# Kernel optimization log

Hardware: AMD Instinct MI355X
Metric: run time of the kernel (lower is better)

The kernel has to match this reference:

```python
import jax, jax.numpy as jnp
import numpy as np

GAMMA = 0.7
ALPHA = 1.0
EPS = 1e-6

def setup_inputs() -> dict:
    key = jax.random.key(0)
    k1, k2 = jax.random.split(key)
    x = jax.random.normal(k1, (1, 4096, 1024), dtype=jnp.float32)
    attn = jax.random.uniform(k2, (1, 4096, 4096), dtype=jnp.float32)
    return {"x": x, "attn": attn, "layer_idx": 10, "total_layers": 12}


def reference(x, attn, layer_idx, total_layers):
    B, N, D = x.shape  # module's masking/cat logic requires B == 1
    if layer_idx < GAMMA * total_layers:
        return x

    # --- spatial autocorrelation score s ---
    a = x.mean(axis=-1)                                            # [B,N]
    z = (a - a.mean(1, keepdims=True)) / (a.std(1, ddof=1, keepdims=True) + EPS)
    # diag(z z^T * W) == z^2 * diag(W): skip the O(N^2) outer product
    I_l = z * z * jnp.diagonal(attn, axis1=-2, axis2=-1)           # [B,N]
    s = (I_l - I_l.mean(1, keepdims=True)) / (I_l.std(1, ddof=1, keepdims=True) + EPS)

    # --- threshold (torch.median returns the LOWER middle for even N) ---
    mu_s = s.mean(1, keepdims=True)
    abs_med = jnp.sort(jnp.abs(s), axis=1)[:, (N - 1) // 2][:, None]
    lb = ALPHA * (mu_s - abs_med)
    ub = ALPHA * (mu_s + abs_med)
    mask_A = (s < lb) | (s > ub)                                   # [B,N]

    xb = x[0]
    mA = mask_A[0]
    idx = jnp.arange(N)
    n_A = mA.sum()

    # compact A tokens to the front preserving original order
    orderA = jnp.argsort(~mA, stable=True)
    tokA = xb[orderA]                    # first n_A rows are tokens_A, rest are B tokens (masked later)
    mid = n_A // 2
    n2 = n_A - mid                       # number of A2 tokens

    # A1[i] = tokA[i] (valid i < mid); A2[j] = tokA[mid + j] (valid j < n2)
    A2 = jnp.take(tokA, jnp.clip(mid + idx, 0, N - 1), axis=0)     # [N,D] padded
    validA1 = idx < mid
    validA2 = idx < n2

    sim = tokA @ A2.T                                              # [N,N]
    sim = jnp.where(validA2[None, :], sim, -jnp.inf)
    matches = jnp.argmax(sim, axis=1)                              # [N]
    merged = 0.5 * (tokA + A2[matches])
    merged = jnp.where(validA1[:, None], merged, 0.0)              # rows >= mid zeroed

    # residual A2 tokens (not matched by any valid A1 row), compacted and zero-padded
    drop_idx = jnp.where(validA1, matches, N)                      # OOB index dropped
    matched = jnp.zeros(N, bool).at[drop_idx].set(True, mode='drop')
    resid_valid = validA2 & ~matched
    orderR = jnp.argsort(~resid_valid, stable=True)
    residual = jnp.where(resid_valid[orderR][:, None], A2[orderR], 0.0)  # [N,D]

    # B tokens compacted, then merged tokens appended, zero pad to N
    n_B = N - n_A
    orderB = jnp.argsort(mA, stable=True)
    tokB = jnp.where((idx < n_B)[:, None], xb[orderB], 0.0)        # [N,D]
    shift = jnp.clip(idx - n_B, 0, N - 1)
    in_merged = ((idx >= n_B) & (idx < n_B + mid)).astype(xb.dtype)[:, None]
    out = (tokB + in_merged * merged[shift])[None]                 # [1,N,D]
    return out, residual
```

## Files before the change

### kernel.cpp

```cpp
#include <hip/hip_runtime.h>

#define N 4096
#define D 1024
#define EPSF 1e-6f

typedef _Float16 f16;
typedef f16 f16x8 __attribute__((ext_vector_type(8)));
typedef float f32x4 __attribute__((ext_vector_type(4)));
typedef unsigned long long u64;

#define PLANE ((size_t)2048 * 1024)

struct WS {
  int n_A, mid, n2, n_B, n_resid, pad[3];
  float a[N];
  float diag[N];
  int A1idx[N];
  int A2idx[N];
  int Bidx[N];
  int matches[N];
  int residIdx[N];
  u64 bestKey[2048];
};

__device__ __forceinline__ u64 packKey(float v, int j) {
  unsigned u = __float_as_uint(v);
  unsigned m = (u & 0x80000000u) ? ~u : (u | 0x80000000u);
  return ((u64)m << 32) | (unsigned)(~(unsigned)j);
}

__global__ __launch_bounds__(256) void k_prep(const float* __restrict__ x,
                                              const float* __restrict__ attn, WS* ws) {
  int row = blockIdx.x;
  int t = threadIdx.x;
  float4 v = ((const float4*)(x + (size_t)row * D))[t];
  float sm = v.x + v.y + v.z + v.w;
  for (int o = 32; o; o >>= 1) sm += __shfl_down(sm, o, 64);
  __shared__ float w[4];
  if ((t & 63) == 0) w[t >> 6] = sm;
  __syncthreads();
  if (t == 0) {
    ws->a[row] = (w[0] + w[1] + w[2] + w[3]) * (1.0f / D);
    ws->diag[row] = attn[(size_t)row * N + row];
  }
}

__global__ __launch_bounds__(256) void k_mask(WS* ws) {
  __shared__ double dred[4], dred2[4];
  __shared__ float bcast[2];
  __shared__ int hist[256];
  __shared__ int wsum[4];
  __shared__ unsigned sPrefix;
  __shared__ int sRank;
  int tid = threadIdx.x;
  int lane = tid & 63, wv = tid >> 6;

  #pragma unroll
  for (int q = 0; q < 8; q++) ws->bestKey[tid * 8 + q] = 0ull;

  float av[16];
  double s = 0.0, s2 = 0.0;
  #pragma unroll
  for (int q = 0; q < 4; q++) {
    float4 va = ((const float4*)ws->a)[tid * 4 + q];
    float f4[4] = {va.x, va.y, va.z, va.w};
    #pragma unroll
    for (int e = 0; e < 4; e++) {
      av[q * 4 + e] = f4[e];
      s += f4[e]; s2 += (double)f4[e] * f4[e];
    }
  }
  for (int o = 32; o; o >>= 1) { s += __shfl_down(s, o, 64); s2 += __shfl_down(s2, o, 64); }
  if (lane == 0) { dred[wv] = s; dred2[wv] = s2; }
  __syncthreads();
  if (tid == 0) {
    double t1 = dred[0] + dred[1] + dred[2] + dred[3];
    double t2 = dred2[0] + dred2[1] + dred2[2] + dred2[3];
    bcast[0] = (float)(t1 / N);
    bcast[1] = (float)sqrt((t2 - t1 * t1 / N) / (N - 1));
  }
  __syncthreads();
  float meanA = bcast[0], stdA = bcast[1];

  float il[16];
  s = 0.0; s2 = 0.0;
  #pragma unroll
  for (int q = 0; q < 4; q++) {
    float4 dg = ((const float4*)ws->diag)[tid * 4 + q];
    float d4[4] = {dg.x, dg.y, dg.z, dg.w};
    #pragma unroll
    for (int e = 0; e < 4; e++) {
      float z = (av[q * 4 + e] - meanA) / (stdA + EPSF);
      float I = z * z * d4[e];
      il[q * 4 + e] = I;
      s += I; s2 += (double)I * I;
    }
  }
  for (int o = 32; o; o >>= 1) { s += __shfl_down(s, o, 64); s2 += __shfl_down(s2, o, 64); }
  __syncthreads();
  if (lane == 0) { dred[wv] = s; dred2[wv] = s2; }
  __syncthreads();
  if (tid == 0) {
    double t1 = dred[0] + dred[1] + dred[2] + dred[3];
    double t2 = dred2[0] + dred2[1] + dred2[2] + dred2[3];
    bcast[0] = (float)(t1 / N);
    bcast[1] = (float)sqrt((t2 - t1 * t1 / N) / (N - 1));
    sPrefix = 0u; sRank = (N - 1) / 2;
  }
  __syncthreads();
  float meanI = bcast[0], stdI = bcast[1];

  float sv[16]; unsigned ab[16];
  #pragma unroll
  for (int q = 0; q < 16; q++) {
    float sval = (il[q] - meanI) / (stdI + EPSF);
    sv[q] = sval;
    ab[q] = __float_as_uint(fabsf(sval));
  }

  for (int p = 3; p >= 0; p--) {
    hist[tid] = 0;
    __syncthreads();
    unsigned pre = sPrefix;
    int rk = sRank;
    int sh = p * 8;
    unsigned mHi = (p == 3) ? 0u : (0xFFFFFFFFu << (sh + 8));
    #pragma unroll
    for (int q = 0; q < 16; q++)
      if ((ab[q] & mHi) == pre) atomicAdd(&hist[(ab[q] >> sh) & 255], 1);
    __syncthreads();
    int v2 = hist[tid];
    int inc = v2;
    #pragma unroll
    for (int o = 1; o < 64; o <<= 1) { int u = __shfl_up(inc, o, 64); if (lane >= o) inc += u; }
    if (lane == 63) wsum[wv] = inc;
    __syncthreads();
    if (tid == 0) { wsum[1] += wsum[0]; wsum[2] += wsum[1]; wsum[3] += wsum[2]; }
    __syncthreads();
    int incl = (wv ? wsum[wv - 1] : 0) + inc;
    int E = incl - v2;
    if (v2 && rk >= E && rk < E + v2) {
      sPrefix = pre | ((unsigned)tid << sh);
      sRank = rk - E;
    }
    __syncthreads();
  }
  float med = __uint_as_float(sPrefix);

  int msk[16], loc[16]; int tot = 0;
  #pragma unroll
  for (int q = 0; q < 16; q++) {
    bool m = fabsf(sv[q]) > med;
    msk[q] = m; loc[q] = tot; tot += (int)m;
  }
  int inc = tot;
  #pragma unroll
  for (int o = 1; o < 64; o <<= 1) { int u = __shfl_up(inc, o, 64); if (lane >= o) inc += u; }
  if (lane == 63) wsum[wv] = inc;
  __syncthreads();
  if (tid == 0) { wsum[1] += wsum[0]; wsum[2] += wsum[1]; wsum[3] += wsum[2]; }
  __syncthreads();
  int nA = wsum[3];
  int base = (wv ? wsum[wv - 1] : 0) + inc - tot;
  int midl = nA >> 1;
  #pragma unroll
  for (int q = 0; q < 16; q++) {
    int i = tid * 16 + q;
    int r = base + loc[q];
    if (msk[q]) {
      if (r < midl) ws->A1idx[r] = i; else ws->A2idx[r - midl] = i;
    } else {
      ws->Bidx[i - r] = i;
    }
  }
  if (tid == 0) { ws->n_A = nA; ws->mid = midl; ws->n2 = nA - midl; ws->n_B = N - nA; }
}

__global__ __launch_bounds__(128) void k_pack(const float* __restrict__ x,
                                              f16* __restrict__ PAhi, f16* __restrict__ PAlo,
                                              f16* __restrict__ PBhi, f16* __restrict__ PBlo,
                                              WS* ws) {
  int b = blockIdx.x, t = threadIdx.x;
  const float* src;
  f16 *dh, *dl;
  int j;
  if (b < 2048) {
    if (b >= ws->mid) return;
    j = b;
    src = x + (size_t)ws->A1idx[b] * D;
    dh = PAhi; dl = PAlo;
  } else {
    j = b - 2048;
    if (j >= ws->n2) return;
    src = x + (size_t)ws->A2idx[j] * D;
    dh = PBhi; dl = PBlo;
  }
  float4 v0 = ((const float4*)src)[t * 2];
  float4 v1 = ((const float4*)src)[t * 2 + 1];
  float vv[8] = {v0.x, v0.y, v0.z, v0.w, v1.x, v1.y, v1.z, v1.w};
  f16x8 h, l;
  #pragma unroll
  for (int q = 0; q < 8; q++) {
    f16 hq = (f16)vv[q];
    h[q] = hq;
    l[q] = (f16)(vv[q] - (float)hq);
  }
  int rt = j >> 6, rl = j & 63;
  int kt = t >> 3, gl = t & 7;
  size_t off = ((size_t)(rt * 16 + kt) << 12) + rl * 64 + ((gl ^ (rl & 7)) * 8);
  *(f16x8*)(dh + off) = h;
  *(f16x8*)(dl + off) = l;
}

__global__ __launch_bounds__(256) void k_gemm(const f16* __restrict__ PAhi,
                                              const f16* __restrict__ PAlo,
                                              const f16* __restrict__ PBhi,
                                              const f16* __restrict__ PBlo, WS* ws) {
  const int mid = ws->mid, n2 = ws->n2;
  int L = blockIdx.x;
  int local = L >> 3;
  int bj = ((L & 7) << 1) | (local >> 4);
  int bi = local & 15;
  if (bi * 64 >= mid || bj * 64 >= n2) return;

  __shared__ f16 lds[2][4][64 * 64];

  const int tid = threadIdx.x;
  const int lane = tid & 63;
  const int wid = tid >> 6;
  const int wr = wid >> 1, wc = wid & 1;

  const f16* plane = (wid == 0) ? PAhi : (wid == 1) ? PAlo : (wid == 2) ? PBhi : PBlo;
  const int ptile = (wid < 2) ? bi : bj;

  f16x8 pr[8];
  auto LOAD = [&](int t) {
    const f16* tb = plane + ((size_t)((ptile << 4) + t) << 12);
    #pragma unroll
    for (int i = 0; i < 8; i++) pr[i] = *(const f16x8*)(tb + i * 512 + lane * 8);
  };
  auto STORE = [&](int buf) {
    #pragma unroll
    for (int i = 0; i < 8; i++) *(f16x8*)&lds[buf][wid][i * 512 + lane * 8] = pr[i];
  };

  const int colg = lane & 15, rowg = lane >> 4;
  const int ma0 = wr * 32 + colg, ma1 = ma0 + 16;
  const int mb0 = wc * 32 + colg, mb1 = mb0 + 16;

  f32x4 zero = {0.f, 0.f, 0.f, 0.f};
  f32x4 acc[2][2];
  acc[0][0] = zero; acc[0][1] = zero; acc[1][0] = zero; acc[1][1] = zero;

#define FRAG(buf, t4, row, g) \
  (*(const f16x8*)&lds[buf][t4][(row) * 64 + ((((g) ^ ((row) & 7))) * 8)])

  LOAD(0);
  STORE(0);
  __syncthreads();
  for (int t16 = 0; t16 < 16; t16++) {
    int buf = t16 & 1;
    if (t16 < 15) LOAD(t16 + 1);
    #pragma unroll
    for (int ks = 0; ks < 2; ks++) {
      int gk = ks * 4 + rowg;
      f16x8 ah0 = FRAG(buf, 0, ma0, gk), ah1 = FRAG(buf, 0, ma1, gk);
      f16x8 al0 = FRAG(buf, 1, ma0, gk), al1 = FRAG(buf, 1, ma1, gk);
      f16x8 bh0 = FRAG(buf, 2, mb0, gk), bh1 = FRAG(buf, 2, mb1, gk);
      f16x8 bl0 = FRAG(buf, 3, mb0, gk), bl1 = FRAG(buf, 3, mb1, gk);
      acc[0][0] = __builtin_amdgcn_mfma_f32_16x16x32_f16(ah0, bh0, acc[0][0], 0, 0, 0);
      acc[0][0] = __builtin_amdgcn_mfma_f32_16x16x32_f16(ah0, bl0, acc[0][0], 0, 0, 0);
      acc[0][0] = __builtin_amdgcn_mfma_f32_16x16x32_f16(al0, bh0, acc[0][0], 0, 0, 0);
      acc[0][1] = __builtin_amdgcn_mfma_f32_16x16x32_f16(ah0, bh1, acc[0][1], 0, 0, 0);
      acc[0][1] = __builtin_amdgcn_mfma_f32_16x16x32_f16(ah0, bl1, acc[0][1], 0, 0, 0);
      acc[0][1] = __builtin_amdgcn_mfma_f32_16x16x32_f16(al0, bh1, acc[0][1], 0, 0, 0);
      acc[1][0] = __builtin_amdgcn_mfma_f32_16x16x32_f16(ah1, bh0, acc[1][0], 0, 0, 0);
      acc[1][0] = __builtin_amdgcn_mfma_f32_16x16x32_f16(ah1, bl0, acc[1][0], 0, 0, 0);
      acc[1][0] = __builtin_amdgcn_mfma_f32_16x16x32_f16(al1, bh0, acc[1][0], 0, 0, 0);
      acc[1][1] = __builtin_amdgcn_mfma_f32_16x16x32_f16(ah1, bh1, acc[1][1], 0, 0, 0);
      acc[1][1] = __builtin_amdgcn_mfma_f32_16x16x32_f16(ah1, bl1, acc[1][1], 0, 0, 0);
      acc[1][1] = __builtin_amdgcn_mfma_f32_16x16x32_f16(al1, bh1, acc[1][1], 0, 0, 0);
    }
    if (t16 < 15) {
      __syncthreads();
      STORE(buf ^ 1);
      __syncthreads();
    }
  }
#undef FRAG

  #pragma unroll
  for (int mi = 0; mi < 2; mi++) {
    #pragma unroll
    for (int i = 0; i < 4; i++) {
      int grow = bi * 64 + wr * 32 + mi * 16 + rowg * 4 + i;
      u64 key = 0;
      #pragma unroll
      for (int ni = 0; ni < 2; ni++) {
        int gcol = bj * 64 + wc * 32 + ni * 16 + colg;
        if (gcol < n2) {
          u64 k2 = packKey(acc[mi][ni][i], gcol);
          if (k2 > key) key = k2;
        }
      }
      #pragma unroll
      for (int m = 8; m; m >>= 1) {
        u64 o = (u64)__shfl_xor((long long)key, m, 64);
        if (o > key) key = o;
      }
      if (colg == 0 && grow < mid && key) atomicMax(&ws->bestKey[grow], key);
    }
  }
}

__global__ __launch_bounds__(1024) void k_match(WS* ws) {
  __shared__ int flag[N];
  __shared__ int wsum[16];
  int tid = threadIdx.x;
  int lane = tid & 63, wv = tid >> 6;
  int mid = ws->mid, n2 = ws->n2;
  #pragma unroll
  for (int q = 0; q < 4; q++) flag[tid * 4 + q] = 0;
  __syncthreads();
  #pragma unroll
  for (int q = 0; q < 2; q++) {
    int r = tid + q * 1024;
    if (r < mid) {
      int j = (int)(~(unsigned)(ws->bestKey[r] & 0xffffffffull));
      ws->matches[r] = j;
      flag[j] = 1;
    }
  }
  __syncthreads();
  int v[4], loc[4]; int tot = 0;
  #pragma unroll
  for (int q = 0; q < 4; q++) {
    int j = tid * 4 + q;
    bool val = (j < n2) && (flag[j] == 0);
    v[q] = val; loc[q] = tot; tot += (int)val;
  }
  int inc = tot;
  #pragma unroll
  for (int o = 1; o < 64; o <<= 1) { int u = __shfl_up(inc, o, 64); if (lane >= o) inc += u; }
  if (lane == 63) wsum[wv] = inc;
  __syncthreads();
  if (tid < 16) {
    int t = wsum[tid];
    #pragma unroll
    for (int o = 1; o < 16; o <<= 1) { int u = __shfl_up(t, o, 64); if (tid >= o) t += u; }
    wsum[tid] = t;
  }
  __syncthreads();
  int base = (wv ? wsum[wv - 1] : 0) + inc - tot;
  #pragma unroll
  for (int q = 0; q < 4; q++)
    if (v[q]) ws->residIdx[base + loc[q]] = ws->A2idx[tid * 4 + q];
  if (tid == 0) ws->n_resid = wsum[15];
}

__global__ __launch_bounds__(256) void k_write(const float* __restrict__ x,
                                               float* __restrict__ out, WS* ws) {
  int r = blockIdx.x;
  int t = threadIdx.x;
  int n_B = ws->n_B, mid = ws->mid, n_resid = ws->n_resid;
  float4 res = make_float4(0.f, 0.f, 0.f, 0.f);
  if (r < N) {
    if (r < n_B) {
      res = ((const float4*)(x + (size_t)ws->Bidx[r] * D))[t];
    } else if (r < n_B + mid) {
      int m = r - n_B;
      float4 v1 = ((const float4*)(x + (size_t)ws->A1idx[m] * D))[t];
      float4 v2 = ((const float4*)(x + (size_t)ws->A2idx[ws->matches[m]] * D))[t];
      res = make_float4(0.5f * (v1.x + v2.x), 0.5f * (v1.y + v2.y),
                        0.5f * (v1.z + v2.z), 0.5f * (v1.w + v2.w));
    }
  } else {
    int k = r - N;
    if (k < n_resid) {
      res = ((const float4*)(x + (size_t)ws->residIdx[k] * D))[t];
    }
  }
  ((float4*)(out + (size_t)r * D))[t] = res;
}

extern "C" void kernel_launch(void* const* d_in, const int* in_sizes, int n_in,
                              void* d_out, int out_size, void* d_ws, size_t ws_size,
                              hipStream_t stream) {
  const float* x = (const float*)d_in[0];
  const float* attn = (const float*)d_in[1];
  float* out = (float*)d_out;
  WS* ws = (WS*)d_ws;
  f16* PAhi = (f16*)d_out;
  f16* PAlo = PAhi + PLANE;
  f16* PBhi = PAlo + PLANE;
  f16* PBlo = PBhi + PLANE;

  k_prep<<<N, 256, 0, stream>>>(x, attn, ws);
  k_mask<<<1, 256, 0, stream>>>(ws);
  k_pack<<<4096, 128, 0, stream>>>(x, PAhi, PAlo, PBhi, PBlo, ws);
  k_gemm<<<256, 256, 0, stream>>>(PAhi, PAlo, PBhi, PBlo, ws);
  k_match<<<1, 1024, 0, stream>>>(ws);
  k_write<<<2 * N, 256, 0, stream>>>(x, out, ws);
}
```

Measured before the change: 58.18 us.

## Fuse single-block mask and match kernels into preceding kernels via last-block counters

Removes the separate k_mask and k_match launches. Instead, the last block to finish k_prep (and k_gemm) is detected with an atomic counter and a threadfence, and it runs the serial reduction or scan inline. This cuts two kernel launches and their inter-kernel gaps, at the cost of an extra memset, atomic reads of the workspace, and a serial tail that now runs inside a single block of the larger kernel.

```diff
diff --git a/kernel.cpp b/kernel.cpp
--- a/kernel.cpp
+++ b/kernel.cpp
@@ -12,6 +12,7 @@
 #define PLANE ((size_t)2048 * 1024)
 
 struct WS {
+  unsigned c1, c2, c3, c4;
   int n_A, mid, n2, n_B, n_resid, pad[3];
   float a[N];
   float diag[N];
@@ -32,43 +33,45 @@
 __global__ __launch_bounds__(256) void k_prep(const float* __restrict__ x,
                                               const float* __restrict__ attn, WS* ws) {
   int row = blockIdx.x;
-  int t = threadIdx.x;
-  float4 v = ((const float4*)(x + (size_t)row * D))[t];
+  int tid = threadIdx.x;
+  int lane = tid & 63, wv = tid >> 6;
+  __shared__ float w[4];
+  __shared__ int slast;
+
+  float4 v = ((const float4*)(x + (size_t)row * D))[tid];
   float sm = v.x + v.y + v.z + v.w;
   for (int o = 32; o; o >>= 1) sm += __shfl_down(sm, o, 64);
-  __shared__ float w[4];
-  if ((t & 63) == 0) w[t >> 6] = sm;
-  __syncthreads();
-  if (t == 0) {
-    ws->a[row] = (w[0] + w[1] + w[2] + w[3]) * (1.0f / D);
-    ws->diag[row] = attn[(size_t)row * N + row];
-  }
-}
-
-__global__ __launch_bounds__(256) void k_mask(WS* ws) {
+  if (lane == 0) w[wv] = sm;
+  __syncthreads();
+  if (tid == 0) {
+    float am = (w[0] + w[1] + w[2] + w[3]) * (1.0f / D);
+    atomicExch((unsigned*)&ws->a[row], __float_as_uint(am));
+    atomicExch((unsigned*)&ws->diag[row], __float_as_uint(attn[(size_t)row * (N + 1)]));
+    __threadfence();
+    unsigned c = atomicAdd(&ws->c1, 1u);
+    slast = (c == (unsigned)(N - 1));
+  }
+  __syncthreads();
+  if (!slast) return;
+
   __shared__ double dred[4], dred2[4];
   __shared__ float bcast[2];
   __shared__ int hist[256];
   __shared__ int wsum[4];
   __shared__ unsigned sPrefix;
   __shared__ int sRank;
-  int tid = threadIdx.x;
-  int lane = tid & 63, wv = tid >> 6;
 
   #pragma unroll
   for (int q = 0; q < 8; q++) ws->bestKey[tid * 8 + q] = 0ull;
 
-  float av[16];
+  float av[16], dg[16];
   double s = 0.0, s2 = 0.0;
   #pragma unroll
-  for (int q = 0; q < 4; q++) {
-    float4 va = ((const float4*)ws->a)[tid * 4 + q];
-    float f4[4] = {va.x, va.y, va.z, va.w};
-    #pragma unroll
-    for (int e = 0; e < 4; e++) {
-      av[q * 4 + e] = f4[e];
-      s += f4[e]; s2 += (double)f4[e] * f4[e];
-    }
+  for (int q = 0; q < 16; q++) {
+    int i = tid * 16 + q;
+    av[q] = __uint_as_float(atomicOr((unsigned*)&ws->a[i], 0u));
+    dg[q] = __uint_as_float(atomicOr((unsigned*)&ws->diag[i], 0u));
+    s += av[q]; s2 += (double)av[q] * av[q];
   }
   for (int o = 32; o; o >>= 1) { s += __shfl_down(s, o, 64); s2 += __shfl_down(s2, o, 64); }
   if (lane == 0) { dred[wv] = s; dred2[wv] = s2; }
@@ -85,16 +88,10 @@
   float il[16];
   s = 0.0; s2 = 0.0;
   #pragma unroll
-  for (int q = 0; q < 4; q++) {
-    float4 dg = ((const float4*)ws->diag)[tid * 4 + q];
-    float d4[4] = {dg.x, dg.y, dg.z, dg.w};
-    #pragma unroll
-    for (int e = 0; e < 4; e++) {
-      float z = (av[q * 4 + e] - meanA) / (stdA + EPSF);
-      float I = z * z * d4[e];
-      il[q * 4 + e] = I;
-      s += I; s2 += (double)I * I;
-    }
+  for (int q = 0; q < 16; q++) {
+    float z = (av[q] - meanA) / (stdA + EPSF);
+    float I = z * z * dg[q];
+    il[q] = I; s += I; s2 += (double)I * I;
   }
   for (int o = 32; o; o >>= 1) { s += __shfl_down(s, o, 64); s2 += __shfl_down(s2, o, 64); }
   __syncthreads();
@@ -216,146 +213,152 @@
                                               const f16* __restrict__ PAlo,
                                               const f16* __restrict__ PBhi,
                                               const f16* __restrict__ PBlo, WS* ws) {
+  __shared__ __align__(16) f16 lds[2][4][64 * 64];
+  __shared__ int isLast;
+
   const int mid = ws->mid, n2 = ws->n2;
-  int L = blockIdx.x;
-  int local = L >> 3;
-  int bj = ((L & 7) << 1) | (local >> 4);
-  int bi = local & 15;
-  if (bi * 64 >= mid || bj * 64 >= n2) return;
-
-  __shared__ f16 lds[2][4][64 * 64];
-
   const int tid = threadIdx.x;
   const int lane = tid & 63;
-  const int wid = tid >> 6;
-  const int wr = wid >> 1, wc = wid & 1;
-
-  const f16* plane = (wid == 0) ? PAhi : (wid == 1) ? PAlo : (wid == 2) ? PBhi : PBlo;
-  const int ptile = (wid < 2) ? bi : bj;
-
-  f16x8 pr[8];
-  auto LOAD = [&](int t) {
-    const f16* tb = plane + ((size_t)((ptile << 4) + t) << 12);
-    #pragma unroll
-    for (int i = 0; i < 8; i++) pr[i] = *(const f16x8*)(tb + i * 512 + lane * 8);
-  };
-  auto STORE = [&](int buf) {
-    #pragma unroll
-    for (int i = 0; i < 8; i++) *(f16x8*)&lds[buf][wid][i * 512 + lane * 8] = pr[i];
-  };
-
-  const int colg = lane & 15, rowg = lane >> 4;
-  const int ma0 = wr * 32 + colg, ma1 = ma0 + 16;
-  const int mb0 = wc * 32 + colg, mb1 = mb0 + 16;
-
-  f32x4 zero = {0.f, 0.f, 0.f, 0.f};
-  f32x4 acc[2][2];
-  acc[0][0] = zero; acc[0][1] = zero; acc[1][0] = zero; acc[1][1] = zero;
+
+  {
+    int L = blockIdx.x;
+    int local = L >> 3;
+    int bj = ((L & 7) << 1) | (local >> 4);
+    int bi = local & 15;
+    if (bi * 64 < mid && bj * 64 < n2) {
+      const int wid = tid >> 6;
+      const int wr = wid >> 1, wc = wid & 1;
+      const f16* plane = (wid == 0) ? PAhi : (wid == 1) ? PAlo : (wid == 2) ? PBhi : PBlo;
+      const int ptile = (wid < 2) ? bi : bj;
+
+      f16x8 pr[8];
+      auto LOAD = [&](int t) {
+        const f16* tb = plane + ((size_t)((ptile << 4) + t) << 12);
+        #pragma unroll
+        for (int i = 0; i < 8; i++) pr[i] = *(const f16x8*)(tb + i * 512 + lane * 8);
+      };
+      auto STORE = [&](int buf) {
+        #pragma unroll
+        for (int i = 0; i < 8; i++) *(f16x8*)&lds[buf][wid][i * 512 + lane * 8] = pr[i];
+      };
+
+      const int colg = lane & 15, rowg = lane >> 4;
+      const int ma0 = wr * 32 + colg, ma1 = ma0 + 16;
+      const int mb0 = wc * 32 + colg, mb1 = mb0 + 16;
+
+      f32x4 zero = {0.f, 0.f, 0.f, 0.f};
+      f32x4 acc[2][2];
+      acc[0][0] = zero; acc[0][1] = zero; acc[1][0] = zero; acc[1][1] = zero;
 
 #define FRAG(buf, t4, row, g) \
   (*(const f16x8*)&lds[buf][t4][(row) * 64 + ((((g) ^ ((row) & 7))) * 8)])
 
-  LOAD(0);
-  STORE(0);
-  __syncthreads();
-  for (int t16 = 0; t16 < 16; t16++) {
-    int buf = t16 & 1;
-    if (t16 < 15) LOAD(t16 + 1);
-    #pragma unroll
-    for (int ks = 0; ks < 2; ks++) {
-      int gk = ks * 4 + rowg;
-      f16x8 ah0 = FRAG(buf, 0, ma0, gk), ah1 = FRAG(buf, 0, ma1, gk);
-      f16x8 al0 = FRAG(buf, 1, ma0, gk), al1 = FRAG(buf, 1, ma1, gk);
-      f16x8 bh0 = FRAG(buf, 2, mb0, gk), bh1 = FRAG(buf, 2, mb1, gk);
-      f16x8 bl0 = FRAG(buf, 3, mb0, gk), bl1 = FRAG(buf, 3, mb1, gk);
-      acc[0][0] = __builtin_amdgcn_mfma_f32_16x16x32_f16(ah0, bh0, acc[0][0], 0, 0, 0);
-      acc[0][0] = __builtin_amdgcn_mfma_f32_16x16x32_f16(ah0, bl0, acc[0][0], 0, 0, 0);
-      acc[0][0] = __builtin_amdgcn_mfma_f32_16x16x32_f16(al0, bh0, acc[0][0], 0, 0, 0);
-      acc[0][1] = __builtin_amdgcn_mfma_f32_16x16x32_f16(ah0, bh1, acc[0][1], 0, 0, 0);
-      acc[0][1] = __builtin_amdgcn_mfma_f32_16x16x32_f16(ah0, bl1, acc[0][1], 0, 0, 0);
-      acc[0][1] = __builtin_amdgcn_mfma_f32_16x16x32_f16(al0, bh1, acc[0][1], 0, 0, 0);
-      acc[1][0] = __builtin_amdgcn_mfma_f32_16x16x32_f16(ah1, bh0, acc[1][0], 0, 0, 0);
-      acc[1][0] = __builtin_amdgcn_mfma_f32_16x16x32_f16(ah1, bl0, acc[1][0], 0, 0, 0);
-      acc[1][0] = __builtin_amdgcn_mfma_f32_16x16x32_f16(al1, bh0, acc[1][0], 0, 0, 0);
-      acc[1][1] = __builtin_amdgcn_mfma_f32_16x16x32_f16(ah1, bh1, acc[1][1], 0, 0, 0);
-      acc[1][1] = __builtin_amdgcn_mfma_f32_16x16x32_f16(ah1, bl1, acc[1][1], 0, 0, 0);
-      acc[1][1] = __builtin_amdgcn_mfma_f32_16x16x32_f16(al1, bh1, acc[1][1], 0, 0, 0);
-    }
-    if (t16 < 15) {
+      LOAD(0);
+      STORE(0);
       __syncthreads();
-      STORE(buf ^ 1);
-      __syncthreads();
-    }
-  }
-#undef FRAG
-
-  #pragma unroll
-  for (int mi = 0; mi < 2; mi++) {
-    #pragma unroll
-    for (int i = 0; i < 4; i++) {
-      int grow = bi * 64 + wr * 32 + mi * 16 + rowg * 4 + i;
-      u64 key = 0;
-      #pragma unroll
-      for (int ni = 0; ni < 2; ni++) {
-        int gcol = bj * 64 + wc * 32 + ni * 16 + colg;
-        if (gcol < n2) {
-          u64 k2 = packKey(acc[mi][ni][i], gcol);
-          if (k2 > key) key = k2;
+      #pragma unroll 1
+      for (int t16 = 0; t16 < 16; t16++) {
+        int buf = t16 & 1;
+        if (t16 < 15) LOAD(t16 + 1);
+        #pragma unroll
+        for (int ks = 0; ks < 2; ks++) {
+          int gk = ks * 4 + rowg;
+          f16x8 ah0 = FRAG(buf, 0, ma0, gk), ah1 = FRAG(buf, 0, ma1, gk);
+          f16x8 al0 = FRAG(buf, 1, ma0, gk), al1 = FRAG(buf, 1, ma1, gk);
+          f16x8 bh0 = FRAG(buf, 2, mb0, gk), bh1 = FRAG(buf, 2, mb1, gk);
+          f16x8 bl0 = FRAG(buf, 3, mb0, gk), bl1 = FRAG(buf, 3, mb1, gk);
+          acc[0][0] = __builtin_amdgcn_mfma_f32_16x16x32_f16(ah0, bh0, acc[0][0], 0, 0, 0);
+          acc[0][0] = __builtin_amdgcn_mfma_f32_16x16x32_f16(ah0, bl0, acc[0][0], 0, 0, 0);
+          acc[0][0] = __builtin_amdgcn_mfma_f32_16x16x32_f16(al0, bh0, acc[0][0], 0, 0, 0);
+          acc[0][1] = __builtin_amdgcn_mfma_f32_16x16x32_f16(ah0, bh1, acc[0][1], 0, 0, 0);
+          acc[0][1] = __builtin_amdgcn_mfma_f32_16x16x32_f16(ah0, bl1, acc[0][1], 0, 0, 0);
+          acc[0][1] = __builtin_amdgcn_mfma_f32_16x16x32_f16(al0, bh1, acc[0][1], 0, 0, 0);
+          acc[1][0] = __builtin_amdgcn_mfma_f32_16x16x32_f16(ah1, bh0, acc[1][0], 0, 0, 0);
+          acc[1][0] = __builtin_amdgcn_mfma_f32_16x16x32_f16(ah1, bl0, acc[1][0], 0, 0, 0);
+          acc[1][0] = __builtin_amdgcn_mfma_f32_16x16x32_f16(al1, bh0, acc[1][0], 0, 0, 0);
+          acc[1][1] = __builtin_amdgcn_mfma_f32_16x16x32_f16(ah1, bh1, acc[1][1], 0, 0, 0);
+          acc[1][1] = __builtin_amdgcn_mfma_f32_16x16x32_f16(ah1, bl1, acc[1][1], 0, 0, 0);
+          acc[1][1] = __builtin_amdgcn_mfma_f32_16x16x32_f16(al1, bh1, acc[1][1], 0, 0, 0);
+        }
+        if (t16 < 15) {
+          __syncthreads();
+          STORE(buf ^ 1);
+          __syncthreads();
         }
       }
+#undef FRAG
+
       #pragma unroll
-      for (int m = 8; m; m >>= 1) {
-        u64 o = (u64)__shfl_xor((long long)key, m, 64);
-        if (o > key) key = o;
+      for (int mi = 0; mi < 2; mi++) {
+        #pragma unroll
+        for (int i = 0; i < 4; i++) {
+          int grow = bi * 64 + wr * 32 + mi * 16 + rowg * 4 + i;
+          u64 key = 0;
+          #pragma unroll
+          for (int ni = 0; ni < 2; ni++) {
+            int gcol = bj * 64 + wc * 32 + ni * 16 + colg;
+            if (gcol < n2) {
+              u64 k2 = packKey(acc[mi][ni][i], gcol);
+              if (k2 > key) key = k2;
+            }
+          }
+          #pragma unroll
+          for (int m = 8; m; m >>= 1) {
+            u64 o = (u64)__shfl_xor((long long)key, m, 64);
+            if (o > key) key = o;
+          }
+          if (colg == 0 && grow < mid && key) atomicMax(&ws->bestKey[grow], key);
+        }
       }
-      if (colg == 0 && grow < mid && key) atomicMax(&ws->bestKey[grow], key);
-    }
-  }
-}
-
-__global__ __launch_bounds__(1024) void k_match(WS* ws) {
-  __shared__ int flag[N];
-  __shared__ int wsum[16];
-  int tid = threadIdx.x;
-  int lane = tid & 63, wv = tid >> 6;
-  int mid = ws->mid, n2 = ws->n2;
-  #pragma unroll
-  for (int q = 0; q < 4; q++) flag[tid * 4 + q] = 0;
-  __syncthreads();
-  #pragma unroll
-  for (int q = 0; q < 2; q++) {
-    int r = tid + q * 1024;
-    if (r < mid) {
-      int j = (int)(~(unsigned)(ws->bestKey[r] & 0xffffffffull));
-      ws->matches[r] = j;
-      flag[j] = 1;
-    }
-  }
-  __syncthreads();
-  int v[4], loc[4]; int tot = 0;
-  #pragma unroll
-  for (int q = 0; q < 4; q++) {
-    int j = tid * 4 + q;
-    bool val = (j < n2) && (flag[j] == 0);
-    v[q] = val; loc[q] = tot; tot += (int)val;
-  }
-  int inc = tot;
-  #pragma unroll
-  for (int o = 1; o < 64; o <<= 1) { int u = __shfl_up(inc, o, 64); if (lane >= o) inc += u; }
-  if (lane == 63) wsum[wv] = inc;
-  __syncthreads();
-  if (tid < 16) {
-    int t = wsum[tid];
-    #pragma unroll
-    for (int o = 1; o < 16; o <<= 1) { int u = __shfl_up(t, o, 64); if (tid >= o) t += u; }
-    wsum[tid] = t;
-  }
-  __syncthreads();
-  int base = (wv ? wsum[wv - 1] : 0) + inc - tot;
-  #pragma unroll
-  for (int q = 0; q < 4; q++)
-    if (v[q]) ws->residIdx[base + loc[q]] = ws->A2idx[tid * 4 + q];
-  if (tid == 0) ws->n_resid = wsum[15];
+    }
+  }
+  __syncthreads();
+  if (tid == 0) {
+    __threadfence();
+    unsigned c = atomicAdd(&ws->c3, 1u);
+    isLast = (c == 255u);
+  }
+  __syncthreads();
+  if (!isLast) return;
+
+  {
+    int* flag = (int*)lds;
+    int* mwsum = flag + N;
+    int wv = tid >> 6;
+    #pragma unroll
+    for (int q = 0; q < 16; q++) flag[tid * 16 + q] = 0;
+    __syncthreads();
+    #pragma unroll
+    for (int q = 0; q < 8; q++) {
+      int r = tid + q * 256;
+      if (r < mid) {
+        u64 k = atomicMax(&ws->bestKey[r], 0ull);
+        int j = (int)(~(unsigned)(k & 0xffffffffull));
+        ws->matches[r] = j;
+        flag[j] = 1;
+      }
+    }
+    __syncthreads();
+    int v[8], loc[8]; int tot = 0;
+    #pragma unroll
+    for (int q = 0; q < 8; q++) {
+      int j = tid * 8 + q;
+      bool val = (j < ws->n2) && (flag[j] == 0);
+      v[q] = val; loc[q] = tot; tot += (int)val;
+    }
+    int inc = tot;
+    #pragma unroll
+    for (int o = 1; o < 64; o <<= 1) { int u = __shfl_up(inc, o, 64); if (lane >= o) inc += u; }
+    if (lane == 63) mwsum[wv] = inc;
+    __syncthreads();
+    if (tid == 0) { mwsum[1] += mwsum[0]; mwsum[2] += mwsum[1]; mwsum[3] += mwsum[2]; }
+    __syncthreads();
+    int base = (wv ? mwsum[wv - 1] : 0) + inc - tot;
+    #pragma unroll
+    for (int q = 0; q < 8; q++)
+      if (v[q]) ws->residIdx[base + loc[q]] = ws->A2idx[tid * 8 + q];
+    if (tid == 0) ws->n_resid = mwsum[3];
+  }
 }
 
 __global__ __launch_bounds__(256) void k_write(const float* __restrict__ x,
@@ -395,10 +398,9 @@
   f16* PBhi = PAlo + PLANE;
   f16* PBlo = PBhi + PLANE;
 
+  hipMemsetAsync(&ws->c1, 0, 4 * sizeof(unsigned), stream);
   k_prep<<<N, 256, 0, stream>>>(x, attn, ws);
-  k_mask<<<1, 256, 0, stream>>>(ws);
   k_pack<<<4096, 128, 0, stream>>>(x, PAhi, PAlo, PBhi, PBlo, ws);
   k_gemm<<<256, 256, 0, stream>>>(PAhi, PAlo, PBhi, PBlo, ws);
-  k_match<<<1, 1024, 0, stream>>>(ws);
   k_write<<<2 * N, 256, 0, stream>>>(x, out, ws);
 }
```

Measured after the change: 146.5 us. 152% more time.
